# Kernel tuning notes

Hardware: AMD Instinct MI355X
Metric: run time of the kernel (lower is better)

The kernel has to match this reference:

```python
import jax, jax.numpy as jnp
import numpy as np

RATIO = 0.2
OLD_CL = 11

def setup_inputs() -> dict:
    key = jax.random.key(0)
    inputs = jax.random.normal(key, (8, 19, 512, 1024), dtype=jnp.float32)
    return {"inputs": inputs}

def reference(inputs):
    N, C, H, W = inputs.shape
    probs = jax.nn.softmax(inputs, axis=1)              # (N,C,H,W)
    argpred = jnp.argmax(probs, axis=1)                 # (N,H,W) int
    # Per-image class histogram via one segment_sum: segment id = n*C + class
    flat = argpred.reshape(N, H * W)
    ids = (flat + (jnp.arange(N, dtype=flat.dtype)[:, None] * C)).reshape(-1)
    hist = jax.ops.segment_sum(jnp.ones((N * H * W,), jnp.float32), ids,
                               num_segments=N * C).reshape(N, C)
    hist = jnp.where(hist == 0, 1.0, hist)              # hist[hist==0]=1
    weight = jnp.power(hist.sum(axis=1, keepdims=True) / hist, RATIO)  # (N,C)
    if OLD_CL > 0:
        weight = weight.at[:, :OLD_CL].set(1.0)
    weight = jax.lax.stop_gradient(weight)[:, :, None, None]  # (N,C,1,1), detached
    loss = -(probs * probs) * weight
    return loss.mean()
```

## Files before the change

kernel.cpp:

```cpp
#include <hip/hip_runtime.h>

#define NIMG 8
#define NC 19
#define HW (512*1024)
#define BPI 128
#define TPB 256
#define ITERS 4
#define OLD_CL 11

__global__ __launch_bounds__(TPB) void iw_main(const float* __restrict__ in,
                                               float* __restrict__ sPart,
                                               unsigned* __restrict__ hPart) {
    const int b   = blockIdx.x;
    const int n   = b >> 7;
    const int bl  = b & (BPI - 1);
    const int tid = threadIdx.x;
    const float* img = in + (size_t)n * NC * HW;

    float    acc[NC];
    unsigned hc[NC];
#pragma unroll
    for (int c = 0; c < NC; ++c) { acc[c] = 0.f; hc[c] = 0u; }

    const float L2E = 1.4426950408889634f;

    for (int it = 0; it < ITERS; ++it) {
        const int    chunk = (bl * TPB + tid) + it * (BPI * TPB);
        const size_t p     = (size_t)chunk * 4;

        float x0[NC], x1[NC], x2[NC], x3[NC];
#pragma unroll
        for (int c = 0; c < NC; ++c) {
            const float4 t = *reinterpret_cast<const float4*>(img + (size_t)c * HW + p);
            x0[c] = t.x; x1[c] = t.y; x2[c] = t.z; x3[c] = t.w;
        }

#define PIXEL(X)                                                            \
        {                                                                   \
            float m = X[0]; int mi = 0;                                     \
            _Pragma("unroll")                                               \
            for (int c = 1; c < NC; ++c) {                                  \
                const bool g = X[c] > m;                                    \
                m  = g ? X[c] : m;                                          \
                mi = g ? c    : mi;                                         \
            }                                                               \
            _Pragma("unroll")                                               \
            for (int c = 0; c < NC; ++c) hc[c] += (mi == c) ? 1u : 0u;      \
            const float ml = m * L2E;                                       \
            float e[NC]; float d = 0.f;                                     \
            _Pragma("unroll")                                               \
            for (int c = 0; c < NC; ++c) {                                  \
                e[c] = exp2f(fmaf(X[c], L2E, -ml));                         \
                d += e[c];                                                  \
            }                                                               \
            const float inv  = 1.0f / d;                                    \
            const float inv2 = inv * inv;                                   \
            _Pragma("unroll")                                               \
            for (int c = 0; c < NC; ++c)                                    \
                acc[c] = fmaf(e[c] * e[c], inv2, acc[c]);                   \
        }

        PIXEL(x0); PIXEL(x1); PIXEL(x2); PIXEL(x3);
#undef PIXEL
    }

#pragma unroll
    for (int c = 0; c < NC; ++c) {
#pragma unroll
        for (int off = 32; off >= 1; off >>= 1) {
            acc[c] += __shfl_xor(acc[c], off, 64);
            hc[c]  += (unsigned)__shfl_xor((int)hc[c], off, 64);
        }
    }

    __shared__ float    ls[TPB / 64][NC];
    __shared__ unsigned lh[TPB / 64][NC];
    const int wave = tid >> 6;
    const int lane = tid & 63;
    if (lane == 0) {
#pragma unroll
        for (int c = 0; c < NC; ++c) { ls[wave][c] = acc[c]; lh[wave][c] = hc[c]; }
    }
    __syncthreads();
    if (tid < NC) {
        float s = 0.f; unsigned h = 0u;
#pragma unroll
        for (int w = 0; w < TPB / 64; ++w) { s += ls[w][tid]; h += lh[w][tid]; }
        sPart[(size_t)b * NC + tid] = s;
        hPart[(size_t)b * NC + tid] = h;
    }
}

__global__ __launch_bounds__(256) void iw_final(const float* __restrict__ sPart,
                                                const unsigned* __restrict__ hPart,
                                                float* __restrict__ out) {
    __shared__ double contrib[NIMG * NC];
    __shared__ double histL[NIMG * NC];
    __shared__ double hsum[NIMG];
    const int t = threadIdx.x;

    double S = 0.0, H = 0.0;
    if (t < NIMG * NC) {
        const int n = t / NC, c = t % NC;
        double s = 0.0; unsigned h = 0u;
        for (int j = 0; j < BPI; ++j) {
            s += (double)sPart[(size_t)(n * BPI + j) * NC + c];
            h += hPart[(size_t)(n * BPI + j) * NC + c];
        }
        H = (h == 0u) ? 1.0 : (double)h;
        S = s;
        histL[t] = H;
    }
    __syncthreads();
    if (t < NIMG) {
        double hs = 0.0;
        for (int c = 0; c < NC; ++c) hs += histL[t * NC + c];
        hsum[t] = hs;
    }
    __syncthreads();
    if (t < NIMG * NC) {
        const int n = t / NC, c = t % NC;
        const double w = (c < OLD_CL) ? 1.0 : pow(hsum[n] / H, 0.2);
        contrib[t] = w * S;
    } else if (t < 256) {
    }
    __syncthreads();
    if (t == 0) {
        double tot = 0.0;
        for (int i = 0; i < NIMG * NC; ++i) tot += contrib[i];
        out[0] = (float)(-tot / (double)((size_t)NIMG * NC * HW));
    }
}

extern "C" void kernel_launch(void* const* d_in, const int* in_sizes, int n_in,
                              void* d_out, int out_size, void* d_ws, size_t ws_size,
                              hipStream_t stream) {
    const float* in = (const float*)d_in[0];
    float* out = (float*)d_out;

    float*    sPart = (float*)d_ws;
    unsigned* hPart = (unsigned*)((char*)d_ws + (size_t)NIMG * BPI * NC * sizeof(float));

    iw_main<<<dim3(NIMG * BPI), TPB, 0, stream>>>(in, sPart, hPart);
    iw_final<<<1, 256, 0, stream>>>(sPart, hPart, out);
}
```

Measured before the change: 72.36 us.

## Pack histogram counters, recompute squared probs via exp2, double grid and split final reduce

Doubles blocks per image and halves iterations, adds an occupancy hint to launch bounds, and packs the per-class argmax counts into three 4-bit-field registers instead of 19 counters. Argmax becomes fmax followed by a first-equal search. The squared probability is computed directly as exp2(2x·log2e − 2m − 2·log2 d), so the e[] array no longer has to stay live, at the cost of 19 extra exp2 per pixel. The final kernel splits each partial-sum reduction across 4 threads. Each thread handles 8 pixels, so the 4-bit fields cannot overflow.

```diff
diff --git a/kernel.cpp b/kernel.cpp
--- a/kernel.cpp
+++ b/kernel.cpp
@@ -3,26 +3,28 @@
 #define NIMG 8
 #define NC 19
 #define HW (512*1024)
-#define BPI 128
+#define BPI 256
 #define TPB 256
-#define ITERS 4
+#define ITERS 2
 #define OLD_CL 11
 
-__global__ __launch_bounds__(TPB) void iw_main(const float* __restrict__ in,
-                                               float* __restrict__ sPart,
-                                               unsigned* __restrict__ hPart) {
+__global__ __launch_bounds__(TPB, 4) void iw_main(const float* __restrict__ in,
+                                                  float* __restrict__ sPart,
+                                                  unsigned* __restrict__ hPart) {
     const int b   = blockIdx.x;
-    const int n   = b >> 7;
+    const int n   = b >> 8;
     const int bl  = b & (BPI - 1);
     const int tid = threadIdx.x;
     const float* img = in + (size_t)n * NC * HW;
 
     float    acc[NC];
-    unsigned hc[NC];
+    unsigned hc[3];
 #pragma unroll
-    for (int c = 0; c < NC; ++c) { acc[c] = 0.f; hc[c] = 0u; }
+    for (int c = 0; c < NC; ++c) acc[c] = 0.f;
+    hc[0] = hc[1] = hc[2] = 0u;
 
-    const float L2E = 1.4426950408889634f;
+    const float L2E  = 1.4426950408889634f;
+    const float L2E2 = 2.8853900817779268f;
 
     for (int it = 0; it < ITERS; ++it) {
         const int    chunk = (bl * TPB + tid) + it * (BPI * TPB);
@@ -35,41 +37,50 @@
             x0[c] = t.x; x1[c] = t.y; x2[c] = t.z; x3[c] = t.w;
         }
 
-#define PIXEL(X)                                                            \
-        {                                                                   \
-            float m = X[0]; int mi = 0;                                     \
-            _Pragma("unroll")                                               \
-            for (int c = 1; c < NC; ++c) {                                  \
-                const bool g = X[c] > m;                                    \
-                m  = g ? X[c] : m;                                          \
-                mi = g ? c    : mi;                                         \
-            }                                                               \
-            _Pragma("unroll")                                               \
-            for (int c = 0; c < NC; ++c) hc[c] += (mi == c) ? 1u : 0u;      \
-            const float ml = m * L2E;                                       \
-            float e[NC]; float d = 0.f;                                     \
-            _Pragma("unroll")                                               \
-            for (int c = 0; c < NC; ++c) {                                  \
-                e[c] = exp2f(fmaf(X[c], L2E, -ml));                         \
-                d += e[c];                                                  \
-            }                                                               \
-            const float inv  = 1.0f / d;                                    \
-            const float inv2 = inv * inv;                                   \
-            _Pragma("unroll")                                               \
-            for (int c = 0; c < NC; ++c)                                    \
-                acc[c] = fmaf(e[c] * e[c], inv2, acc[c]);                   \
+#define PIXEL(X)                                                              \
+        {                                                                     \
+                                                       \
+            float m = X[0];                                                   \
+            _Pragma("unroll")                                                 \
+            for (int c = 1; c < NC; ++c) m = fmaxf(m, X[c]);                  \
+                  \
+            int mi = NC - 1;                                                  \
+            _Pragma("unroll")                                                 \
+            for (int c = NC - 2; c >= 0; --c) mi = (X[c] == m) ? c : mi;      \
+                             \
+            {                                                                 \
+                const unsigned inc = 1u << ((mi & 7) * 4);                    \
+                const int r = mi >> 3;                                        \
+                hc[0] += (r == 0) ? inc : 0u;                                 \
+                hc[1] += (r == 1) ? inc : 0u;                                 \
+                hc[2] += (r == 2) ? inc : 0u;                                 \
+            }                                                                 \
+            const float ml = m * L2E;                                         \
+            float d = 0.f;                                                    \
+            _Pragma("unroll")                                                 \
+            for (int c = 0; c < NC; ++c)                                      \
+                d += exp2f(fmaf(X[c], L2E, -ml));                             \
+                            \
+            const float h = fmaf(-2.f, __log2f(d), -2.f * ml);                \
+            _Pragma("unroll")                                                 \
+            for (int c = 0; c < NC; ++c)                                      \
+                acc[c] += exp2f(fmaf(X[c], L2E2, h));                         \
         }
 
         PIXEL(x0); PIXEL(x1); PIXEL(x2); PIXEL(x3);
 #undef PIXEL
     }
 
+    unsigned hu[NC];
+#pragma unroll
+    for (int c = 0; c < NC; ++c) hu[c] = (hc[c >> 3] >> ((c & 7) * 4)) & 0xFu;
+
 #pragma unroll
     for (int c = 0; c < NC; ++c) {
 #pragma unroll
         for (int off = 32; off >= 1; off >>= 1) {
             acc[c] += __shfl_xor(acc[c], off, 64);
-            hc[c]  += (unsigned)__shfl_xor((int)hc[c], off, 64);
+            hu[c]  += (unsigned)__shfl_xor((int)hu[c], off, 64);
         }
     }
 
@@ -79,7 +90,7 @@
     const int lane = tid & 63;
     if (lane == 0) {
 #pragma unroll
-        for (int c = 0; c < NC; ++c) { ls[wave][c] = acc[c]; lh[wave][c] = hc[c]; }
+        for (int c = 0; c < NC; ++c) { ls[wave][c] = acc[c]; lh[wave][c] = hu[c]; }
     }
     __syncthreads();
     if (tid < NC) {
@@ -91,25 +102,34 @@
     }
 }
 
-__global__ __launch_bounds__(256) void iw_final(const float* __restrict__ sPart,
-                                                const unsigned* __restrict__ hPart,
-                                                float* __restrict__ out) {
+__global__ __launch_bounds__(1024) void iw_final(const float* __restrict__ sPart,
+                                                 const unsigned* __restrict__ hPart,
+                                                 float* __restrict__ out) {
+    __shared__ double   ps[NIMG * NC][4];
+    __shared__ unsigned ph[NIMG * NC][4];
     __shared__ double contrib[NIMG * NC];
     __shared__ double histL[NIMG * NC];
     __shared__ double hsum[NIMG];
-    const int t = threadIdx.x;
+    const int t   = threadIdx.x;
+    const int idx = t >> 2;
+    const int k   = t & 3;
 
-    double S = 0.0, H = 0.0;
-    if (t < NIMG * NC) {
-        const int n = t / NC, c = t % NC;
+    if (idx < NIMG * NC) {
+        const int n = idx / NC, c = idx % NC;
         double s = 0.0; unsigned h = 0u;
-        for (int j = 0; j < BPI; ++j) {
+        for (int j = k; j < BPI; j += 4) {
             s += (double)sPart[(size_t)(n * BPI + j) * NC + c];
             h += hPart[(size_t)(n * BPI + j) * NC + c];
         }
-        H = (h == 0u) ? 1.0 : (double)h;
-        S = s;
+        ps[idx][k] = s; ph[idx][k] = h;
+    }
+    __syncthreads();
+    if (t < NIMG * NC) {
+        double s = ps[t][0] + ps[t][1] + ps[t][2] + ps[t][3];
+        unsigned h = ph[t][0] + ph[t][1] + ph[t][2] + ph[t][3];
+        const double H = (h == 0u) ? 1.0 : (double)h;
         histL[t] = H;
+        contrib[t] = s;
     }
     __syncthreads();
     if (t < NIMG) {
@@ -120,9 +140,8 @@
     __syncthreads();
     if (t < NIMG * NC) {
         const int n = t / NC, c = t % NC;
-        const double w = (c < OLD_CL) ? 1.0 : pow(hsum[n] / H, 0.2);
-        contrib[t] = w * S;
-    } else if (t < 256) {
+        const double w = (c < OLD_CL) ? 1.0 : pow(hsum[n] / histL[t], 0.2);
+        contrib[t] = w * contrib[t];
     }
     __syncthreads();
     if (t == 0) {
@@ -142,5 +161,5 @@
     unsigned* hPart = (unsigned*)((char*)d_ws + (size_t)NIMG * BPI * NC * sizeof(float));
 
     iw_main<<<dim3(NIMG * BPI), TPB, 0, stream>>>(in, sPart, hPart);
-    iw_final<<<1, 256, 0, stream>>>(sPart, hPart, out);
+    iw_final<<<1, 1024, 0, stream>>>(sPart, hPart, out);
 }
```

Result: slower. 101.7 us (+40.5%).
